# Kernel optimization log

Hardware: AMD Instinct MI355X
Metric: run time of the kernel (lower is better)

## Reference

```python
import jax, jax.numpy as jnp
import numpy as np


def setup_inputs() -> dict:
    key = jax.random.key(0)
    k1, k2, k3, k4 = jax.random.split(key, 4)
    N, H, C, D = 65536, 1024, 1000, 8192
    seq_feats = jax.random.normal(k1, (N, H), dtype=jnp.float32)
    seq_logits = jax.random.normal(k2, (N, C), dtype=jnp.float32)
    W_attn = jax.random.normal(k3, (H, 1), dtype=jnp.float32) * 0.02
    b_attn = jnp.zeros((1,), dtype=jnp.float32)
    doc_label_mask = jnp.ones((C,), dtype=jnp.float32)
    segment_ids = jnp.sort(jax.random.randint(k4, (N,), 0, D, dtype=jnp.int32))
    return {
        "seq_feats": seq_feats,
        "seq_logits": seq_logits,
        "W_attn": W_attn,
        "b_attn": b_attn,
        "doc_label_mask": doc_label_mask,
        "segment_ids": segment_ids,
        "num_docs": D,
    }


def reference(seq_feats, seq_logits, W_attn, b_attn, doc_label_mask, segment_ids, num_docs):
    # attention scores per sentence: [N]
    scores = (seq_feats @ W_attn + b_attn)[:, 0]
    # numerically-stable per-document softmax via segment reductions
    seg_max = jax.ops.segment_max(scores, segment_ids, num_segments=num_docs)  # [D]
    ex = jnp.exp(scores - seg_max[segment_ids])                                # [N]
    denom = jax.ops.segment_sum(ex, segment_ids, num_segments=num_docs)        # [D]
    w = ex / denom[segment_ids]                                                # [N]
    # softmax-weighted sum of sentence logits per document: [D, C]
    doc_logits = jax.ops.segment_sum(w[:, None] * seq_logits, segment_ids,
                                     num_segments=num_docs)
    # doc label mask offset (mask==1 -> no-op, mask==0 -> -1e10)
    doc_logits = doc_logits + (doc_label_mask[None, :] - 1.0) * 1e10
    return doc_logits
```

## Files before the change

### kernel.cpp

```cpp
#include <hip/hip_runtime.h>
#include <math.h>
#include <float.h>

__global__ void start_kernel(const int* __restrict__ seg,
                             int* __restrict__ start, int N, int D) {
    int d = blockIdx.x * blockDim.x + threadIdx.x;
    if (d > D) return;
    int lo = 0, hi = N;
    while (lo < hi) {
        int mid = (lo + hi) >> 1;
        if (seg[mid] < d) lo = mid + 1; else hi = mid;
    }
    start[d] = lo;
}

__global__ __launch_bounds__(256) void scoresex_kernel(
    const float* __restrict__ feats,
    const float* __restrict__ Wv,
    const float* __restrict__ bv,
    float* __restrict__ ex,
    int N, int H) {

    const int lane = threadIdx.x & 63;
    const int wave = threadIdx.x >> 6;
    const int r0 = blockIdx.x * 8 + wave * 2;
    const int r1 = r0 + 1;
    const int nvh = H >> 2;
    const float4* w4 = reinterpret_cast<const float4*>(Wv);

    float4 wr[4];
    #pragma unroll
    for (int k = 0; k < 4; ++k) {
        int idx = lane + 64 * k;
        wr[k] = (idx < nvh) ? w4[idx] : make_float4(0.f, 0.f, 0.f, 0.f);
    }
    const float bias = bv[0];

    if (r0 >= N) return;
    const float4* f0 = reinterpret_cast<const float4*>(feats + (size_t)r0 * H);
    const float4* f1 = reinterpret_cast<const float4*>(feats + (size_t)((r1 < N) ? r1 : r0) * H);

    float4 a0[4], a1[4];
    #pragma unroll
    for (int k = 0; k < 4; ++k) {
        int idx = lane + 64 * k;
        if (idx < nvh) { a0[k] = f0[idx]; a1[k] = f1[idx]; }
        else { a0[k] = make_float4(0.f,0.f,0.f,0.f); a1[k] = make_float4(0.f,0.f,0.f,0.f); }
    }
    float p0 = 0.f, p1 = 0.f;
    #pragma unroll
    for (int k = 0; k < 4; ++k) {
        p0 += a0[k].x * wr[k].x + a0[k].y * wr[k].y + a0[k].z * wr[k].z + a0[k].w * wr[k].w;
        p1 += a1[k].x * wr[k].x + a1[k].y * wr[k].y + a1[k].z * wr[k].z + a1[k].w * wr[k].w;
    }
    for (int idx = lane + 256; idx < nvh; idx += 64) {
        float4 w = w4[idx];
        float4 b0 = f0[idx]; p0 += b0.x*w.x + b0.y*w.y + b0.z*w.z + b0.w*w.w;
        float4 b1 = f1[idx]; p1 += b1.x*w.x + b1.y*w.y + b1.z*w.z + b1.w*w.w;
    }
    #pragma unroll
    for (int off = 32; off > 0; off >>= 1) {
        p0 += __shfl_xor(p0, off, 64);
        p1 += __shfl_xor(p1, off, 64);
    }
    if (lane == 0) {
        ex[r0] = __expf(p0 + bias);
        if (r1 < N) ex[r1] = __expf(p1 + bias);
    }
}

__global__ __launch_bounds__(256) void docsum_kernel(
    const float* __restrict__ logits,
    const float* __restrict__ ex,
    const int* __restrict__ start,
    const float* __restrict__ mask,
    float* __restrict__ out, int C) {

    const int d = blockIdx.x;
    const int t = threadIdx.x;
    const int nvc = C >> 2;
    const int s = start[d];
    const int e = start[d + 1];
    const float4* l4 = reinterpret_cast<const float4*>(logits);

    float4 acc = make_float4(0.f, 0.f, 0.f, 0.f);
    if (t < nvc) {
        int j = s;
        for (; j + 1 < e; j += 2) {
            const float e0 = ex[j], e1 = ex[j + 1];
            float4 v0 = l4[(size_t)j * nvc + t];
            float4 v1 = l4[(size_t)(j + 1) * nvc + t];
            acc.x += e0 * v0.x + e1 * v1.x;
            acc.y += e0 * v0.y + e1 * v1.y;
            acc.z += e0 * v0.z + e1 * v1.z;
            acc.w += e0 * v0.w + e1 * v1.w;
        }
        if (j < e) {
            const float e0 = ex[j];
            float4 v0 = l4[(size_t)j * nvc + t];
            acc.x += e0 * v0.x; acc.y += e0 * v0.y;
            acc.z += e0 * v0.z; acc.w += e0 * v0.w;
        }
    }

    float den = 0.f;
    for (int i = s; i < e; ++i) den += ex[i];
    const float r = (e > s) ? (1.0f / den) : 0.f;

    if (t < nvc) {
        float4 mm = reinterpret_cast<const float4*>(mask)[t];
        float4 o;
        o.x = acc.x * r + (mm.x - 1.f) * 1e10f;
        o.y = acc.y * r + (mm.y - 1.f) * 1e10f;
        o.z = acc.z * r + (mm.z - 1.f) * 1e10f;
        o.w = acc.w * r + (mm.w - 1.f) * 1e10f;
        reinterpret_cast<float4*>(out)[(size_t)d * nvc + t] = o;
    }
}

extern "C" void kernel_launch(void* const* d_in, const int* in_sizes, int n_in,
                              void* d_out, int out_size, void* d_ws, size_t ws_size,
                              hipStream_t stream) {
    const float* seq_feats  = (const float*)d_in[0];
    const float* seq_logits = (const float*)d_in[1];
    const float* W_attn     = (const float*)d_in[2];
    const float* b_attn     = (const float*)d_in[3];
    const float* mask       = (const float*)d_in[4];
    const int*   seg        = (const int*)d_in[5];

    int H = in_sizes[2];
    int C = in_sizes[4];
    int N = in_sizes[5];
    int D = out_size / C;

    int*   start = (int*)d_ws;
    float* ex    = (float*)(start + (D + 1) + 3);

    start_kernel<<<(D + 1 + 255) / 256, 256, 0, stream>>>(seg, start, N, D);
    scoresex_kernel<<<(N + 7) / 8, 256, 0, stream>>>(seq_feats, W_attn, b_attn,
                                                     ex, N, H);
    docsum_kernel<<<D, 256, 0, stream>>>(seq_logits, ex, start, mask,
                                         (float*)d_out, C);
}
```

Measured before the change: 123.4 us.

## Fuse segment bounds, score/exp, and weighted doc sum into one kernel

Replaces the three kernels (binary-search start offsets, per-row score+exp, per-document weighted sum) with one kernel in which each block handles two documents. The block computes its own segment bounds, scores the rows in chunks into shared memory, then accumulates logits and denominators from shared memory. This drops the ex round-trip through global memory and two kernel launches. In exchange the grid shrinks to D/2 blocks, and score computation now alternates with accumulation behind block barriers, which may reduce latency hiding.

```diff
diff --git a/kernel.cpp b/kernel.cpp
--- a/kernel.cpp
+++ b/kernel.cpp
@@ -2,31 +2,41 @@
 #include <math.h>
 #include <float.h>
 
-__global__ void start_kernel(const int* __restrict__ seg,
-                             int* __restrict__ start, int N, int D) {
-    int d = blockIdx.x * blockDim.x + threadIdx.x;
-    if (d > D) return;
-    int lo = 0, hi = N;
-    while (lo < hi) {
-        int mid = (lo + hi) >> 1;
-        if (seg[mid] < d) lo = mid + 1; else hi = mid;
-    }
-    start[d] = lo;
-}
+#define DPB   2
+#define CHUNK 96
 
-__global__ __launch_bounds__(256) void scoresex_kernel(
+__global__ __launch_bounds__(256) void fused_kernel(
     const float* __restrict__ feats,
     const float* __restrict__ Wv,
     const float* __restrict__ bv,
-    float* __restrict__ ex,
-    int N, int H) {
+    const float* __restrict__ logits,
+    const int* __restrict__ seg,
+    const float* __restrict__ mask,
+    float* __restrict__ out,
+    int N, int H, int C, int D) {
 
-    const int lane = threadIdx.x & 63;
-    const int wave = threadIdx.x >> 6;
-    const int r0 = blockIdx.x * 8 + wave * 2;
-    const int r1 = r0 + 1;
+    const int t = threadIdx.x;
+    const int lane = t & 63;
+    const int wave = t >> 6;
+    const int g0 = blockIdx.x * DPB;
+
+    __shared__ int   sb[DPB + 1];
+    __shared__ float sx[CHUNK];
+
+    if (t <= DPB) {
+        int dq = g0 + t; if (dq > D) dq = D;
+        int lo = 0, hi = N;
+        while (lo < hi) {
+            int mid = (lo + hi) >> 1;
+            if (seg[mid] < dq) lo = mid + 1; else hi = mid;
+        }
+        sb[t] = lo;
+    }
+
     const int nvh = H >> 2;
+    const int nvc = C >> 2;
     const float4* w4 = reinterpret_cast<const float4*>(Wv);
+    const float4* l4 = reinterpret_cast<const float4*>(logits);
 
     float4 wr[4];
     #pragma unroll
@@ -36,85 +46,99 @@
     }
     const float bias = bv[0];
 
-    if (r0 >= N) return;
-    const float4* f0 = reinterpret_cast<const float4*>(feats + (size_t)r0 * H);
-    const float4* f1 = reinterpret_cast<const float4*>(feats + (size_t)((r1 < N) ? r1 : r0) * H);
+    __syncthreads();
+    int bnd[DPB + 1];
+    #pragma unroll
+    for (int dd = 0; dd <= DPB; ++dd) bnd[dd] = sb[dd];
+    const int s = bnd[0], e = bnd[DPB];
 
-    float4 a0[4], a1[4];
+    float4 acc[DPB];
+    float  den[DPB];
     #pragma unroll
-    for (int k = 0; k < 4; ++k) {
-        int idx = lane + 64 * k;
-        if (idx < nvh) { a0[k] = f0[idx]; a1[k] = f1[idx]; }
-        else { a0[k] = make_float4(0.f,0.f,0.f,0.f); a1[k] = make_float4(0.f,0.f,0.f,0.f); }
-    }
-    float p0 = 0.f, p1 = 0.f;
-    #pragma unroll
-    for (int k = 0; k < 4; ++k) {
-        p0 += a0[k].x * wr[k].x + a0[k].y * wr[k].y + a0[k].z * wr[k].z + a0[k].w * wr[k].w;
-        p1 += a1[k].x * wr[k].x + a1[k].y * wr[k].y + a1[k].z * wr[k].z + a1[k].w * wr[k].w;
-    }
-    for (int idx = lane + 256; idx < nvh; idx += 64) {
-        float4 w = w4[idx];
-        float4 b0 = f0[idx]; p0 += b0.x*w.x + b0.y*w.y + b0.z*w.z + b0.w*w.w;
-        float4 b1 = f1[idx]; p1 += b1.x*w.x + b1.y*w.y + b1.z*w.z + b1.w*w.w;
-    }
-    #pragma unroll
-    for (int off = 32; off > 0; off >>= 1) {
-        p0 += __shfl_xor(p0, off, 64);
-        p1 += __shfl_xor(p1, off, 64);
-    }
-    if (lane == 0) {
-        ex[r0] = __expf(p0 + bias);
-        if (r1 < N) ex[r1] = __expf(p1 + bias);
-    }
-}
-
-__global__ __launch_bounds__(256) void docsum_kernel(
-    const float* __restrict__ logits,
-    const float* __restrict__ ex,
-    const int* __restrict__ start,
-    const float* __restrict__ mask,
-    float* __restrict__ out, int C) {
-
-    const int d = blockIdx.x;
-    const int t = threadIdx.x;
-    const int nvc = C >> 2;
-    const int s = start[d];
-    const int e = start[d + 1];
-    const float4* l4 = reinterpret_cast<const float4*>(logits);
-
-    float4 acc = make_float4(0.f, 0.f, 0.f, 0.f);
-    if (t < nvc) {
-        int j = s;
-        for (; j + 1 < e; j += 2) {
-            const float e0 = ex[j], e1 = ex[j + 1];
-            float4 v0 = l4[(size_t)j * nvc + t];
-            float4 v1 = l4[(size_t)(j + 1) * nvc + t];
-            acc.x += e0 * v0.x + e1 * v1.x;
-            acc.y += e0 * v0.y + e1 * v1.y;
-            acc.z += e0 * v0.z + e1 * v1.z;
-            acc.w += e0 * v0.w + e1 * v1.w;
-        }
-        if (j < e) {
-            const float e0 = ex[j];
-            float4 v0 = l4[(size_t)j * nvc + t];
-            acc.x += e0 * v0.x; acc.y += e0 * v0.y;
-            acc.z += e0 * v0.z; acc.w += e0 * v0.w;
-        }
+    for (int dd = 0; dd < DPB; ++dd) {
+        acc[dd] = make_float4(0.f, 0.f, 0.f, 0.f);
+        den[dd] = 0.f;
     }
 
-    float den = 0.f;
-    for (int i = s; i < e; ++i) den += ex[i];
-    const float r = (e > s) ? (1.0f / den) : 0.f;
+    for (int cs = s; cs < e; cs += CHUNK) {
+        const int ce = min(cs + CHUNK, e);
+
+        for (int r0 = cs + wave * 2; r0 < ce; r0 += 8) {
+            const int r1ok = (r0 + 1 < ce);
+            const float4* f0 = reinterpret_cast<const float4*>(feats + (size_t)r0 * H);
+            const float4* f1 = reinterpret_cast<const float4*>(feats + (size_t)(r1ok ? r0 + 1 : r0) * H);
+            float p0 = 0.f, p1 = 0.f;
+            #pragma unroll
+            for (int k = 0; k < 4; ++k) {
+                int idx = lane + 64 * k;
+                if (idx < nvh) {
+                    float4 a0 = f0[idx], a1 = f1[idx];
+                    p0 += a0.x * wr[k].x + a0.y * wr[k].y + a0.z * wr[k].z + a0.w * wr[k].w;
+                    p1 += a1.x * wr[k].x + a1.y * wr[k].y + a1.z * wr[k].z + a1.w * wr[k].w;
+                }
+            }
+            for (int idx = lane + 256; idx < nvh; idx += 64) {
+                float4 w = w4[idx];
+                float4 a0 = f0[idx], a1 = f1[idx];
+                p0 += a0.x * w.x + a0.y * w.y + a0.z * w.z + a0.w * w.w;
+                p1 += a1.x * w.x + a1.y * w.y + a1.z * w.z + a1.w * w.w;
+            }
+            #pragma unroll
+            for (int off = 32; off > 0; off >>= 1) {
+                p0 += __shfl_xor(p0, off, 64);
+                p1 += __shfl_xor(p1, off, 64);
+            }
+            if (lane == 0) {
+                sx[r0 - cs] = __expf(p0 + bias);
+                if (r1ok) sx[r0 + 1 - cs] = __expf(p1 + bias);
+            }
+        }
+        __syncthreads();
+
+        if (t < nvc) {
+            #pragma unroll
+            for (int dd = 0; dd < DPB; ++dd) {
+                const int ds = max(bnd[dd], cs);
+                const int de = min(bnd[dd + 1], ce);
+                int j = ds;
+                for (; j + 3 < de; j += 4) {
+                    const float e0 = sx[j - cs],     e1 = sx[j - cs + 1];
+                    const float e2 = sx[j - cs + 2], e3 = sx[j - cs + 3];
+                    float4 v0 = l4[(size_t)j * nvc + t];
+                    float4 v1 = l4[(size_t)(j + 1) * nvc + t];
+                    float4 v2 = l4[(size_t)(j + 2) * nvc + t];
+                    float4 v3 = l4[(size_t)(j + 3) * nvc + t];
+                    acc[dd].x += e0 * v0.x + e1 * v1.x + e2 * v2.x + e3 * v3.x;
+                    acc[dd].y += e0 * v0.y + e1 * v1.y + e2 * v2.y + e3 * v3.y;
+                    acc[dd].z += e0 * v0.z + e1 * v1.z + e2 * v2.z + e3 * v3.z;
+                    acc[dd].w += e0 * v0.w + e1 * v1.w + e2 * v2.w + e3 * v3.w;
+                }
+                for (; j < de; ++j) {
+                    const float e0 = sx[j - cs];
+                    float4 v0 = l4[(size_t)j * nvc + t];
+                    acc[dd].x += e0 * v0.x; acc[dd].y += e0 * v0.y;
+                    acc[dd].z += e0 * v0.z; acc[dd].w += e0 * v0.w;
+                }
+                for (int i = ds; i < de; ++i) den[dd] += sx[i - cs];
+            }
+        }
+        if (ce < e) __syncthreads();
+    }
 
     if (t < nvc) {
         float4 mm = reinterpret_cast<const float4*>(mask)[t];
-        float4 o;
-        o.x = acc.x * r + (mm.x - 1.f) * 1e10f;
-        o.y = acc.y * r + (mm.y - 1.f) * 1e10f;
-        o.z = acc.z * r + (mm.z - 1.f) * 1e10f;
-        o.w = acc.w * r + (mm.w - 1.f) * 1e10f;
-        reinterpret_cast<float4*>(out)[(size_t)d * nvc + t] = o;
+        #pragma unroll
+        for (int dd = 0; dd < DPB; ++dd) {
+            const int d = g0 + dd;
+            if (d >= D) break;
+            const float r = (bnd[dd + 1] > bnd[dd]) ? (1.0f / den[dd]) : 0.f;
+            float4 o;
+            o.x = acc[dd].x * r + (mm.x - 1.f) * 1e10f;
+            o.y = acc[dd].y * r + (mm.y - 1.f) * 1e10f;
+            o.z = acc[dd].z * r + (mm.z - 1.f) * 1e10f;
+            o.w = acc[dd].w * r + (mm.w - 1.f) * 1e10f;
+            reinterpret_cast<float4*>(out)[(size_t)d * nvc + t] = o;
+        }
     }
 }
 
@@ -133,12 +157,7 @@
     int N = in_sizes[5];
     int D = out_size / C;
 
-    int*   start = (int*)d_ws;
-    float* ex    = (float*)(start + (D + 1) + 3);
-
-    start_kernel<<<(D + 1 + 255) / 256, 256, 0, stream>>>(seg, start, N, D);
-    scoresex_kernel<<<(N + 7) / 8, 256, 0, stream>>>(seq_feats, W_attn, b_attn,
-                                                     ex, N, H);
-    docsum_kernel<<<D, 256, 0, stream>>>(seq_logits, ex, start, mask,
-                                         (float*)d_out, C);
+    int grid = (D + DPB - 1) / DPB;
+    fused_kernel<<<grid, 256, 0, stream>>>(seq_feats, W_attn, b_attn, seq_logits,
+                                           seg, mask, (float*)d_out, N, H, C, D);
 }
```

Measured after the change: 129.9 us. 1.05x slower.
